# Performance work log

Measured on AMD Instinct MI355X. Metric: run time of the kernel, lower is better.

## Reference

```python
import jax, jax.numpy as jnp
import numpy as np

ROI_POOLING_SIZE = 7
CROP = ROI_POOLING_SIZE * 2  # before_pooling_size = 14


def _crop_and_resize(img, boxes, crop):
    """tf.image.crop_and_resize (bilinear, extrapolation_value=0) for a single image.

    img:   [H, W, C]
    boxes: [N, 4] normalized [y1, x1, y2, x2]
    returns [N, crop, crop, C]
    """
    H, W, C = img.shape
    y1, x1, y2, x2 = boxes[:, 0], boxes[:, 1], boxes[:, 2], boxes[:, 3]
    idx = jnp.arange(crop, dtype=img.dtype)  # crop > 1 branch of TF semantics
    # sample coordinates in source-pixel space: [N, crop]
    ys = y1[:, None] * (H - 1) + idx[None, :] * ((y2 - y1) * (H - 1) / (crop - 1))[:, None]
    xs = x1[:, None] * (W - 1) + idx[None, :] * ((x2 - x1) * (W - 1) / (crop - 1))[:, None]

    y0f = jnp.floor(ys)
    x0f = jnp.floor(xs)
    ly = ys - y0f  # bilinear fractional weights [N, crop]
    lx = xs - x0f

    y0 = jnp.clip(y0f.astype(jnp.int32), 0, H - 1)
    y1i = jnp.clip(y0 + 1, 0, H - 1)
    x0 = jnp.clip(x0f.astype(jnp.int32), 0, W - 1)
    x1i = jnp.clip(x0 + 1, 0, W - 1)

    # out-of-image samples get extrapolation_value = 0
    vy = (ys >= 0) & (ys <= H - 1)  # [N, crop]
    vx = (xs >= 0) & (xs <= W - 1)

    # irregular per-box bilinear gather: val[n,i,j,c] = img[y[n,i], x[n,j], c]
    def g(yi, xi):
        return img[yi[:, :, None], xi[:, None, :]]  # [N, crop, crop, C]

    v00 = g(y0, x0)
    v01 = g(y0, x1i)
    v10 = g(y1i, x0)
    v11 = g(y1i, x1i)

    lxb = lx[:, None, :, None]
    lyb = ly[:, :, None, None]
    top = v00 + (v01 - v00) * lxb
    bot = v10 + (v11 - v10) * lxb
    val = top + (bot - top) * lyb

    valid = (vy[:, :, None] & vx[:, None, :])[..., None]
    return jnp.where(valid, val, jnp.zeros((), dtype=img.dtype))


def reference(feature_maps, proposals, image_shape):
    # proposals are pixel-space [x1, y1, x2, y2]; normalize to [y1/h, x1/w, y2/h, x2/w]
    h = image_shape[0].astype(jnp.float32)
    w = image_shape[1].astype(jnp.float32)
    boxes = jnp.stack(
        [proposals[:, 1] / h, proposals[:, 0] / w, proposals[:, 3] / h, proposals[:, 2] / w],
        axis=1,
    )
    crops = _crop_and_resize(feature_maps[0], boxes, CROP)  # [N, 14, 14, C]
    N, Hc, Wc, C = crops.shape
    # MaxPooling2D(pool=2, stride=2, padding='same'); 14 is even so no padding needed
    pooled = crops.reshape(N, Hc // 2, 2, Wc // 2, 2, C).max(axis=(2, 4))
    return pooled  # [N, 7, 7, C]


def setup_inputs() -> dict:
    key = jax.random.key(0)
    k1, k2, k3, k4, k5 = jax.random.split(key, 5)
    H_img, W_img = 800, 1216
    N = 2000
    feature_maps = jax.random.normal(k1, (1, 200, 304, 256), dtype=jnp.float32)
    # realistic boxes in image pixel coords [x1, y1, x2, y2]
    x1 = jax.random.uniform(k2, (N,), minval=0.0, maxval=0.75 * W_img)
    y1 = jax.random.uniform(k3, (N,), minval=0.0, maxval=0.75 * H_img)
    bw = jax.random.uniform(k4, (N,), minval=16.0, maxval=0.25 * W_img)
    bh = jax.random.uniform(k5, (N,), minval=16.0, maxval=0.25 * H_img)
    proposals = jnp.stack([x1, y1, jnp.minimum(x1 + bw, W_img - 1.0), jnp.minimum(y1 + bh, H_img - 1.0)], axis=1).astype(jnp.float32)
    image_shape = jnp.array([H_img, W_img], dtype=jnp.int32)
    return {"feature_maps": feature_maps, "proposals": proposals, "image_shape": image_shape}
```

## Files before the change

kernel.cpp:

```cpp
#include <hip/hip_runtime.h>
#include <math.h>

#define H_FM 200
#define W_FM 304
#define C_FM 256
#define NPIX (H_FM * W_FM)
#define CROP 14
#define PH 7
#define NPOS 49
#define NSAMP (NPOS * 4)
#define SLABS 16
#define SLAB_C 16
#define SLAB_ELEMS (NPIX * SLAB_C)
#define SPIXB (SLAB_C * 4)
#define PIXB (C_FM * 4)
#define GEOM_PER_ROI 28

#define SLAB_BYTES ((size_t)SLABS * SLAB_ELEMS * sizeof(float))

typedef float floatx4 __attribute__((ext_vector_type(4)));

#define TP 16
__global__ __launch_bounds__(256) void repack_kernel(
    const float* __restrict__ fm,
    float*       __restrict__ slabbed)
{
    __shared__ float lds[TP][C_FM + 4];
    const int tid = threadIdx.x;
    const int p0  = blockIdx.x * TP;

    const float4* src = (const float4*)(fm + (size_t)p0 * C_FM);
    #pragma unroll
    for (int i = 0; i < 4; ++i) {
        const int idx = i * 256 + tid;
        const float4 v = src[idx];
        const int pix = idx >> 6;
        const int c4  = idx & 63;
        *(float4*)&lds[pix][c4 * 4] = v;
    }
    __syncthreads();

    const int s = tid >> 4;
    const int j = tid & 15;
    float* dst = slabbed + (size_t)s * SLAB_ELEMS + (size_t)p0 * SLAB_C;
    #pragma unroll
    for (int k = 0; k < 4; ++k) {
        const int m   = k * 16 + j;
        const int pix = m >> 2;
        const int cq  = m & 3;
        const float4 v = *(const float4*)&lds[pix][s * SLAB_C + cq * 4];
        *(float4*)(dst + m * 4) = v;
    }
}

__global__ __launch_bounds__(256, 2) void roi_pool_fused_kernel(
    const float* __restrict__ slabbed,
    const float* __restrict__ proposals,
    const int*   __restrict__ image_shape,
    float*       __restrict__ out,
    int N)
{
    __shared__ uint4 gLds[GEOM_PER_ROI];

    const int bid   = blockIdx.x;
    const int xcd   = bid & 7;
    const int jj    = bid >> 3;
    const int phase = jj / N;
    const int n     = jj - phase * N;
    const int slab  = phase * 8 + xcd;

    const int tid = threadIdx.x;

    if (tid < GEOM_PER_ROI) {
        const int e = tid;

        const float himg = (float)image_shape[0];
        const float wimg = (float)image_shape[1];

        const float bx1 = proposals[n * 4 + 0] / wimg;
        const float by1 = proposals[n * 4 + 1] / himg;
        const float bx2 = proposals[n * 4 + 2] / wimg;
        const float by2 = proposals[n * 4 + 3] / himg;

        const float Hm1 = (float)(H_FM - 1);
        const float Wm1 = (float)(W_FM - 1);

        uint4 ge;
        if (e < CROP) {
            const int i = e;
            const float ystep = (by2 - by1) * Hm1 / (float)(CROP - 1);
            const float ys    = by1 * Hm1 + (float)i * ystep;
            const float y0f   = floorf(ys);
            const float ly    = ys - y0f;
            int y0 = min(max((int)y0f, 0), H_FM - 1);
            const int dy = min(y0 + 1, H_FM - 1) - y0;
            const bool vy = (ys >= 0.0f) && (ys <= Hm1);
            const float vf = vy ? 1.0f : 0.0f;
            ge.x = (uint32_t)(y0 * W_FM) * SPIXB;
            ge.y = __float_as_uint((1.0f - ly) * vf);
            ge.z = __float_as_uint(ly * vf);
            ge.w = (uint32_t)(dy * W_FM) * SPIXB;
        } else {
            const int j = e - CROP;
            const float xstep = (bx2 - bx1) * Wm1 / (float)(CROP - 1);
            const float xs    = bx1 * Wm1 + (float)j * xstep;
            const float x0f   = floorf(xs);
            const float lx    = xs - x0f;
            int x0 = min(max((int)x0f, 0), W_FM - 1);
            const int dx = min(x0 + 1, W_FM - 1) - x0;
            const bool vx = (xs >= 0.0f) && (xs <= Wm1);
            const float vf = vx ? 1.0f : 0.0f;
            ge.x = (uint32_t)x0 * SPIXB;
            ge.y = __float_as_uint((1.0f - lx) * vf);
            ge.z = __float_as_uint(lx * vf);
            ge.w = (uint32_t)dx * SPIXB;
        }
        gLds[e] = ge;
    }
    __syncthreads();

    const int wave = tid >> 6;
    const int lane = tid & 63;
    const int p    = wave * 16 + (lane >> 2);
    const int q    = lane & 3;
    const int pa   = min(p, NPOS - 1);
    const int py   = pa / PH;
    const int px   = pa - py * PH;

    const char* base = (const char*)slabbed + (size_t)slab * (SLAB_ELEMS * sizeof(float));
    const uint32_t qB = (uint32_t)q * 16u;

    const uint4 yg0 = gLds[2 * py];
    const uint4 yg1 = gLds[2 * py + 1];
    const uint4 xg0 = gLds[CROP + 2 * px];
    const uint4 xg1 = gLds[CROP + 2 * px + 1];

#define GEOM_SAMPLE(s, YG, XG) \
    const uint32_t o00_##s = YG.x + XG.x + qB;              \
    const uint32_t o01_##s = o00_##s + XG.w;                \
    const uint32_t o10_##s = o00_##s + YG.w;                \
    const uint32_t o11_##s = o10_##s + XG.w;                \
    const float wt_##s = __uint_as_float(YG.y);             \
    const float wb_##s = __uint_as_float(YG.z);             \
    const float wl_##s = __uint_as_float(XG.y);             \
    const float wr_##s = __uint_as_float(XG.z);             \
    const float w00_##s = wt_##s * wl_##s;                  \
    const float w01_##s = wt_##s * wr_##s;                  \
    const float w10_##s = wb_##s * wl_##s;                  \
    const float w11_##s = wb_##s * wr_##s;

    GEOM_SAMPLE(0, yg0, xg0)
    GEOM_SAMPLE(1, yg0, xg1)
    GEOM_SAMPLE(2, yg1, xg0)
    GEOM_SAMPLE(3, yg1, xg1)
#undef GEOM_SAMPLE

    const float4 t00_0 = *(const float4*)(base + o00_0);
    const float4 t01_0 = *(const float4*)(base + o01_0);
    const float4 t10_0 = *(const float4*)(base + o10_0);
    const float4 t11_0 = *(const float4*)(base + o11_0);
    const float4 t00_1 = *(const float4*)(base + o00_1);
    const float4 t01_1 = *(const float4*)(base + o01_1);
    const float4 t10_1 = *(const float4*)(base + o10_1);
    const float4 t11_1 = *(const float4*)(base + o11_1);
    const float4 t00_2 = *(const float4*)(base + o00_2);
    const float4 t01_2 = *(const float4*)(base + o01_2);
    const float4 t10_2 = *(const float4*)(base + o10_2);
    const float4 t11_2 = *(const float4*)(base + o11_2);
    const float4 t00_3 = *(const float4*)(base + o00_3);
    const float4 t01_3 = *(const float4*)(base + o01_3);
    const float4 t10_3 = *(const float4*)(base + o10_3);
    const float4 t11_3 = *(const float4*)(base + o11_3);

#define BILERP(s) \
    float4 v_##s;                                                               \
    v_##s.x = fmaf(t00_##s.x, w00_##s, fmaf(t01_##s.x, w01_##s,                 \
              fmaf(t10_##s.x, w10_##s, t11_##s.x * w11_##s)));                  \
    v_##s.y = fmaf(t00_##s.y, w00_##s, fmaf(t01_##s.y, w01_##s,                 \
              fmaf(t10_##s.y, w10_##s, t11_##s.y * w11_##s)));                  \
    v_##s.z = fmaf(t00_##s.z, w00_##s, fmaf(t01_##s.z, w01_##s,                 \
              fmaf(t10_##s.z, w10_##s, t11_##s.z * w11_##s)));                  \
    v_##s.w = fmaf(t00_##s.w, w00_##s, fmaf(t01_##s.w, w01_##s,                 \
              fmaf(t10_##s.w, w10_##s, t11_##s.w * w11_##s)));

    BILERP(0)
    BILERP(1)
    BILERP(2)
    BILERP(3)
#undef BILERP

    if (p < NPOS) {
        floatx4 m;
        m.x = fmaxf(fmaxf(v_0.x, v_1.x), fmaxf(v_2.x, v_3.x));
        m.y = fmaxf(fmaxf(v_0.y, v_1.y), fmaxf(v_2.y, v_3.y));
        m.z = fmaxf(fmaxf(v_0.z, v_1.z), fmaxf(v_2.z, v_3.z));
        m.w = fmaxf(fmaxf(v_0.w, v_1.w), fmaxf(v_2.w, v_3.w));
        __builtin_nontemporal_store(m,
            (floatx4*)(out + ((size_t)n * NPOS + p) * C_FM + slab * SLAB_C + q * 4));
    }
}

__global__ __launch_bounds__(256) void roi_pool_direct_kernel(
    const float* __restrict__ fm,
    const float* __restrict__ proposals,
    const int*   __restrict__ image_shape,
    float*       __restrict__ out,
    int N)
{
    __shared__ uint4  gO[NSAMP];
    __shared__ float4 gWf[NSAMP];

    const int n   = blockIdx.x;
    const int tid = threadIdx.x;

    if (tid < NSAMP) {
        const int s  = tid & 3;
        const int p  = tid >> 2;
        const int py = p / PH;
        const int px = p - py * PH;
        const int a  = s >> 1;
        const int b  = s & 1;

        const float himg = (float)image_shape[0];
        const float wimg = (float)image_shape[1];
        const float bx1 = proposals[n * 4 + 0] / wimg;
        const float by1 = proposals[n * 4 + 1] / himg;
        const float bx2 = proposals[n * 4 + 2] / wimg;
        const float by2 = proposals[n * 4 + 3] / himg;

        const float Hm1 = (float)(H_FM - 1);
        const float Wm1 = (float)(W_FM - 1);
        const float ystep = (by2 - by1) * Hm1 / (float)(CROP - 1);
        const float xstep = (bx2 - bx1) * Wm1 / (float)(CROP - 1);
        const float ys = by1 * Hm1 + (float)(2 * py + a) * ystep;
        const float xs = bx1 * Wm1 + (float)(2 * px + b) * xstep;

        const float y0f = floorf(ys);
        const float x0f = floorf(xs);
        const float ly  = ys - y0f;
        const float lx  = xs - x0f;
        int y0 = min(max((int)y0f, 0), H_FM - 1);
        int x0 = min(max((int)x0f, 0), W_FM - 1);
        const int dy = min(y0 + 1, H_FM - 1) - y0;
        const int dx = min(x0 + 1, W_FM - 1) - x0;
        const bool valid = (ys >= 0.0f) && (ys <= Hm1) &&
                           (xs >= 0.0f) && (xs <= Wm1);
        const float vf   = valid ? 1.0f : 0.0f;
        const float omlx = 1.0f - lx;
        const float omly = 1.0f - ly;

        float4 w;
        w.x = omlx * omly * vf;
        w.y = lx   * omly * vf;
        w.z = omlx * ly   * vf;
        w.w = lx   * ly   * vf;

        uint4 o;
        o.x = (uint32_t)(y0 * W_FM + x0) * PIXB;
        o.y = (uint32_t)dx * PIXB;
        o.z = (uint32_t)(dy * W_FM) * PIXB;
        o.w = 0u;
        gO[tid]  = o;
        gWf[tid] = w;
    }
    __syncthreads();

    const int wave = tid >> 6;
    const int lane = tid & 63;
    const uint32_t laneB = (uint32_t)lane * 16u;
    const char* fmB  = (const char*)fm;
    char*       outB = (char*)out + (size_t)n * (NPOS * PIXB);

    const int pbeg = (wave * NPOS) >> 2;
    const int pend = ((wave + 1) * NPOS) >> 2;

    for (int p = pbeg; p < pend; ++p) {
        float4 m;
        #pragma unroll
        for (int s = 0; s < 4; ++s) {
            const uint4  o = gO[p * 4 + s];
            const float4 w = gWf[p * 4 + s];
            const uint32_t o00 = o.x + laneB;
            const float4 t00 = *(const float4*)(fmB + o00);
            const float4 t01 = *(const float4*)(fmB + o00 + o.y);
            const float4 t10 = *(const float4*)(fmB + o00 + o.z);
            const float4 t11 = *(const float4*)(fmB + o00 + o.y + o.z);
            float4 v;
            v.x = fmaf(t00.x, w.x, fmaf(t01.x, w.y, fmaf(t10.x, w.z, t11.x * w.w)));
            v.y = fmaf(t00.y, w.x, fmaf(t01.y, w.y, fmaf(t10.y, w.z, t11.y * w.w)));
            v.z = fmaf(t00.z, w.x, fmaf(t01.z, w.y, fmaf(t10.z, w.z, t11.z * w.w)));
            v.w = fmaf(t00.w, w.x, fmaf(t01.w, w.y, fmaf(t10.w, w.z, t11.w * w.w)));
            if (s == 0) { m = v; }
            else {
                m.x = fmaxf(m.x, v.x); m.y = fmaxf(m.y, v.y);
                m.z = fmaxf(m.z, v.z); m.w = fmaxf(m.w, v.w);
            }
        }
        floatx4 mv;
        mv.x = m.x; mv.y = m.y; mv.z = m.z; mv.w = m.w;
        __builtin_nontemporal_store(mv,
            (floatx4*)(outB + (uint32_t)p * PIXB + laneB));
    }
}

extern "C" void kernel_launch(void* const* d_in, const int* in_sizes, int n_in,
                              void* d_out, int out_size, void* d_ws, size_t ws_size,
                              hipStream_t stream) {
    (void)n_in; (void)out_size;

    const float* fm        = (const float*)d_in[0];
    const float* proposals = (const float*)d_in[1];
    const int*   imshape   = (const int*)d_in[2];
    float* out = (float*)d_out;

    const int N = in_sizes[1] / 4;
    const size_t need_slab = SLAB_BYTES;

    if (ws_size >= need_slab) {
        repack_kernel<<<NPIX / TP, 256, 0, stream>>>(fm, (float*)d_ws);
        roi_pool_fused_kernel<<<SLABS * N, 256, 0, stream>>>(
            (const float*)d_ws, proposals, imshape, out, N);
    } else {
        roi_pool_direct_kernel<<<N, 256, 0, stream>>>(
            fm, proposals, imshape, out, N);
    }
}
```

Baseline: 212.3 us.

## Precompute ROI geometry table and process one ROI per wavefront

Adds a separate kernel that computes per-ROI bilinear sample geometry into a workspace table once, rather than recomputing it in every slab block. The main pooling kernel now assigns one ROI per wavefront, so each block covers eight ROIs per slab instead of one ROI across all four waves. This removes the per-block geometry computation and its block-wide barrier, and cuts the block count. The cost is an extra kernel launch and a global table read, and it needs a larger workspace, falling back to the old path otherwise.

```diff
diff --git a/kernel.cpp b/kernel.cpp
--- a/kernel.cpp
+++ b/kernel.cpp
@@ -20,6 +20,62 @@
 
 typedef float floatx4 __attribute__((ext_vector_type(4)));
 
+__global__ __launch_bounds__(256) void geom_kernel(
+    const float* __restrict__ proposals,
+    const int*   __restrict__ image_shape,
+    uint4*       __restrict__ geomTab,
+    int N)
+{
+    const int g = blockIdx.x * 256 + threadIdx.x;
+    if (g >= N * GEOM_PER_ROI) return;
+
+    const int n = g / GEOM_PER_ROI;
+    const int e = g - n * GEOM_PER_ROI;
+
+    const float himg = (float)image_shape[0];
+    const float wimg = (float)image_shape[1];
+
+    const float bx1 = proposals[n * 4 + 0] / wimg;
+    const float by1 = proposals[n * 4 + 1] / himg;
+    const float bx2 = proposals[n * 4 + 2] / wimg;
+    const float by2 = proposals[n * 4 + 3] / himg;
+
+    const float Hm1 = (float)(H_FM - 1);
+    const float Wm1 = (float)(W_FM - 1);
+
+    uint4 out;
+    if (e < CROP) {
+        const int i = e;
+        const float ystep = (by2 - by1) * Hm1 / (float)(CROP - 1);
+        const float ys    = by1 * Hm1 + (float)i * ystep;
+        const float y0f   = floorf(ys);
+        const float ly    = ys - y0f;
+        int y0 = min(max((int)y0f, 0), H_FM - 1);
+        const int dy = min(y0 + 1, H_FM - 1) - y0;
+        const bool vy = (ys >= 0.0f) && (ys <= Hm1);
+        const float vf = vy ? 1.0f : 0.0f;
+        out.x = (uint32_t)(y0 * W_FM) * SPIXB;
+        out.y = __float_as_uint((1.0f - ly) * vf);
+        out.z = __float_as_uint(ly * vf);
+        out.w = (uint32_t)(dy * W_FM) * SPIXB;
+    } else {
+        const int j = e - CROP;
+        const float xstep = (bx2 - bx1) * Wm1 / (float)(CROP - 1);
+        const float xs    = bx1 * Wm1 + (float)j * xstep;
+        const float x0f   = floorf(xs);
+        const float lx    = xs - x0f;
+        int x0 = min(max((int)x0f, 0), W_FM - 1);
+        const int dx = min(x0 + 1, W_FM - 1) - x0;
+        const bool vx = (xs >= 0.0f) && (xs <= Wm1);
+        const float vf = vx ? 1.0f : 0.0f;
+        out.x = (uint32_t)x0 * SPIXB;
+        out.y = __float_as_uint((1.0f - lx) * vf);
+        out.z = __float_as_uint(lx * vf);
+        out.w = (uint32_t)dx * SPIXB;
+    }
+    geomTab[g] = out;
+}
+
 #define TP 16
 __global__ __launch_bounds__(256) void repack_kernel(
     const float* __restrict__ fm,
@@ -53,6 +109,121 @@
     }
 }
 
+__global__ __launch_bounds__(256, 2) void roi_pool_wave_kernel(
+    const float* __restrict__ slabbed,
+    const uint4* __restrict__ geomTab,
+    float*       __restrict__ out,
+    int N, int NG)
+{
+    __shared__ uint4 gw[4][32];
+
+    const int bid   = blockIdx.x;
+    const int xcd   = bid & 7;
+    const int r     = bid >> 3;
+    const int phase = r / NG;
+    const int g     = r - phase * NG;
+    const int slab  = xcd + 8 * phase;
+
+    const int tid  = threadIdx.x;
+    const int w    = tid >> 6;
+    const int lane = tid & 63;
+    const int pq   = lane >> 2;
+    const int q    = lane & 3;
+    const uint32_t qB = (uint32_t)q * 16u;
+
+    const char* base = (const char*)slabbed + (size_t)slab * (SLAB_ELEMS * sizeof(float));
+
+    #pragma unroll
+    for (int half = 0; half < 2; ++half) {
+        const int n = g * 8 + half * 4 + w;
+        if (n < N) {
+            if (lane < GEOM_PER_ROI) {
+                gw[w][lane] = geomTab[n * GEOM_PER_ROI + lane];
+            }
+            asm volatile("s_waitcnt lgkmcnt(0)" ::: "memory");
+            __builtin_amdgcn_sched_barrier(0);
+
+            #pragma unroll
+            for (int it = 0; it < 4; ++it) {
+                const int p  = it * 16 + pq;
+                const int pa = min(p, NPOS - 1);
+                const int py = pa / PH;
+                const int px = pa - py * PH;
+
+                const uint4 yg0 = gw[w][2 * py];
+                const uint4 yg1 = gw[w][2 * py + 1];
+                const uint4 xg0 = gw[w][CROP + 2 * px];
+                const uint4 xg1 = gw[w][CROP + 2 * px + 1];
+
+#define GEOM_SAMPLE(s, YG, XG) \
+    const uint32_t o00_##s = YG.x + XG.x + qB;              \
+    const uint32_t o01_##s = o00_##s + XG.w;                \
+    const uint32_t o10_##s = o00_##s + YG.w;                \
+    const uint32_t o11_##s = o10_##s + XG.w;                \
+    const float wt_##s = __uint_as_float(YG.y);             \
+    const float wb_##s = __uint_as_float(YG.z);             \
+    const float wl_##s = __uint_as_float(XG.y);             \
+    const float wr_##s = __uint_as_float(XG.z);             \
+    const float w00_##s = wt_##s * wl_##s;                  \
+    const float w01_##s = wt_##s * wr_##s;                  \
+    const float w10_##s = wb_##s * wl_##s;                  \
+    const float w11_##s = wb_##s * wr_##s;
+
+                GEOM_SAMPLE(0, yg0, xg0)
+                GEOM_SAMPLE(1, yg0, xg1)
+                GEOM_SAMPLE(2, yg1, xg0)
+                GEOM_SAMPLE(3, yg1, xg1)
+#undef GEOM_SAMPLE
+
+                const float4 t00_0 = *(const float4*)(base + o00_0);
+                const float4 t01_0 = *(const float4*)(base + o01_0);
+                const float4 t10_0 = *(const float4*)(base + o10_0);
+                const float4 t11_0 = *(const float4*)(base + o11_0);
+                const float4 t00_1 = *(const float4*)(base + o00_1);
+                const float4 t01_1 = *(const float4*)(base + o01_1);
+                const float4 t10_1 = *(const float4*)(base + o10_1);
+                const float4 t11_1 = *(const float4*)(base + o11_1);
+                const float4 t00_2 = *(const float4*)(base + o00_2);
+                const float4 t01_2 = *(const float4*)(base + o01_2);
+                const float4 t10_2 = *(const float4*)(base + o10_2);
+                const float4 t11_2 = *(const float4*)(base + o11_2);
+                const float4 t00_3 = *(const float4*)(base + o00_3);
+                const float4 t01_3 = *(const float4*)(base + o01_3);
+                const float4 t10_3 = *(const float4*)(base + o10_3);
+                const float4 t11_3 = *(const float4*)(base + o11_3);
+
+#define BILERP(s) \
+    float4 v_##s;                                                               \
+    v_##s.x = fmaf(t00_##s.x, w00_##s, fmaf(t01_##s.x, w01_##s,                 \
+              fmaf(t10_##s.x, w10_##s, t11_##s.x * w11_##s)));                  \
+    v_##s.y = fmaf(t00_##s.y, w00_##s, fmaf(t01_##s.y, w01_##s,                 \
+              fmaf(t10_##s.y, w10_##s, t11_##s.y * w11_##s)));                  \
+    v_##s.z = fmaf(t00_##s.z, w00_##s, fmaf(t01_##s.z, w01_##s,                 \
+              fmaf(t10_##s.z, w10_##s, t11_##s.z * w11_##s)));                  \
+    v_##s.w = fmaf(t00_##s.w, w00_##s, fmaf(t01_##s.w, w01_##s,                 \
+              fmaf(t10_##s.w, w10_##s, t11_##s.w * w11_##s)));
+
+                BILERP(0)
+                BILERP(1)
+                BILERP(2)
+                BILERP(3)
+#undef BILERP
+
+                if (p < NPOS) {
+                    floatx4 m;
+                    m.x = fmaxf(fmaxf(v_0.x, v_1.x), fmaxf(v_2.x, v_3.x));
+                    m.y = fmaxf(fmaxf(v_0.y, v_1.y), fmaxf(v_2.y, v_3.y));
+                    m.z = fmaxf(fmaxf(v_0.z, v_1.z), fmaxf(v_2.z, v_3.z));
+                    m.w = fmaxf(fmaxf(v_0.w, v_1.w), fmaxf(v_2.w, v_3.w));
+                    __builtin_nontemporal_store(m,
+                        (floatx4*)(out + ((size_t)n * NPOS + p) * C_FM
+                                   + slab * SLAB_C + q * 4));
+                }
+            }
+        }
+    }
+}
+
 __global__ __launch_bounds__(256, 2) void roi_pool_fused_kernel(
     const float* __restrict__ slabbed,
     const float* __restrict__ proposals,
@@ -73,15 +244,12 @@
 
     if (tid < GEOM_PER_ROI) {
         const int e = tid;
-
         const float himg = (float)image_shape[0];
         const float wimg = (float)image_shape[1];
-
         const float bx1 = proposals[n * 4 + 0] / wimg;
         const float by1 = proposals[n * 4 + 1] / himg;
         const float bx2 = proposals[n * 4 + 2] / wimg;
         const float by2 = proposals[n * 4 + 3] / himg;
-
         const float Hm1 = (float)(H_FM - 1);
         const float Wm1 = (float)(W_FM - 1);
 
@@ -313,10 +481,22 @@
     const int*   imshape   = (const int*)d_in[2];
     float* out = (float*)d_out;
 
-    const int N = in_sizes[1] / 4;
-    const size_t need_slab = SLAB_BYTES;
-
-    if (ws_size >= need_slab) {
+    const int N  = in_sizes[1] / 4;
+    const int NG = (N + 7) / 8;
+    const int ngeom = N * GEOM_PER_ROI;
+
+    const size_t geom_bytes = (size_t)ngeom * sizeof(uint4);
+    const size_t need_slab  = SLAB_BYTES;
+    const size_t need_full  = need_slab + geom_bytes;
+
+    if (ws_size >= need_full) {
+        uint4* geomTab = (uint4*)((char*)d_ws + need_slab);
+        geom_kernel<<<(ngeom + 255) / 256, 256, 0, stream>>>(
+            proposals, imshape, geomTab, N);
+        repack_kernel<<<NPIX / TP, 256, 0, stream>>>(fm, (float*)d_ws);
+        roi_pool_wave_kernel<<<8 * NG * 2, 256, 0, stream>>>(
+            (const float*)d_ws, geomTab, out, N, NG);
+    } else if (ws_size >= need_slab) {
         repack_kernel<<<NPIX / TP, 256, 0, stream>>>(fm, (float*)d_ws);
         roi_pool_fused_kernel<<<SLABS * N, 256, 0, stream>>>(
             (const float*)d_ws, proposals, imshape, out, N);
```

Result: slower. 230.8 us (+8.7%).
